# Performance work log

Measured on AMD Instinct MI355X. Metric: run time of the kernel, lower is better.

## Reference

```python
import jax, jax.numpy as jnp
import numpy as np

INPUT_SIZE = 2048
H1 = 256
H2 = 64
NB = 8
BATCH = 16384


def setup_inputs() -> dict:
    key = jax.random.key(0)
    ks = jax.random.split(key, 8)
    x = jax.random.normal(ks[0], (BATCH, INPUT_SIZE), dtype=jnp.float32)
    bucket_indices = jax.random.randint(ks[1], (BATCH,), 0, NB, dtype=jnp.int32)
    # torch nn.Linear weights: (out_features, in_features), bias: (out_features,)
    def lin(k, fan_in, fan_out):
        kw, kb = jax.random.split(k)
        bound = 1.0 / np.sqrt(fan_in)
        W = jax.random.uniform(kw, (fan_out, fan_in), jnp.float32, -bound, bound)
        b = jax.random.uniform(kb, (fan_out,), jnp.float32, -bound, bound)
        return W, b
    W1, b1 = lin(ks[2], INPUT_SIZE, H1 * NB)
    W2, b2 = lin(ks[3], H1, H2 * NB)
    W3, b3 = lin(ks[4], H2, 1 * NB)
    return {"x": x, "bucket_indices": bucket_indices,
            "W1": W1, "b1": b1, "W2": W2, "b2": b2, "W3": W3, "b3": b3}


def _gather_bucket(all_out, idx, width):
    # all_out: (B, NB*width) -> select per-sample bucket slice -> (B, width)
    B = all_out.shape[0]
    per = all_out.reshape(B, NB, width)
    return jnp.take_along_axis(per, idx[:, None, None], axis=1)[:, 0, :]


def reference(x, bucket_indices, W1, b1, W2, b2, W3, b3):
    idx = bucket_indices.astype(jnp.int32)
    h1_all = x @ W1.T + b1                      # (B, H1*NB)
    h1 = jnp.clip(_gather_bucket(h1_all, idx, H1), 0.0, 1.0)
    h2_all = h1 @ W2.T + b2                     # (B, H2*NB)
    h2 = jnp.clip(_gather_bucket(h2_all, idx, H2), 0.0, 1.0)
    out_all = h2 @ W3.T + b3                    # (B, NB)
    out = _gather_bucket(out_all, idx, 1)       # (B, 1)
    return out[:, :, None]                      # (B, 1, 1) matches unsqueeze(-1)
```

## Files before the change

kernel.cpp:

```cpp
#include <hip/hip_runtime.h>

#define INSZ   2048
#define NH1    256
#define NH2    64
#define NB     8
#define BATCH  16384

#define TS        64
#define MAXTILES  (BATCH / TS)
#define GRIDX     (NB * MAXTILES)

#define W1F_U4   (NB * 64 * 16 * 64)
#define W2F_U4   (NB * 8 * 4 * 64)

#define META_OFF  0
#define ORDER_OFF 1024
#define W1F_OFF   (1024 + BATCH * 4)
#define W2F_OFF   (W1F_OFF + W1F_U4 * 16)
#define WS_NEED   (W2F_OFF + W2F_U4 * 16)

typedef float f4  __attribute__((ext_vector_type(4)));
typedef float f32x4 __attribute__((ext_vector_type(4)));
typedef short bf16x8 __attribute__((ext_vector_type(8)));

__device__ __forceinline__ unsigned short f2bf(float f) {
    unsigned u = __float_as_uint(f);
    u += 0x7fffu + ((u >> 16) & 1u);
    return (unsigned short)(u >> 16);
}
__device__ __forceinline__ float clamp01(float v) { return fminf(fmaxf(v, 0.0f), 1.0f); }
__device__ __forceinline__ unsigned pack2(float a, float b) {
    return (unsigned)f2bf(a) | ((unsigned)f2bf(b) << 16);
}

__device__ __forceinline__ void glds16(const short* gsrc, short* ldst) {
    __builtin_amdgcn_global_load_lds(
        (const __attribute__((address_space(1))) unsigned int*)gsrc,
        (__attribute__((address_space(3))) unsigned int*)ldst, 16, 0, 0);
}


__global__ void k_countscan(const int* __restrict__ idx, int* __restrict__ meta) {
    __shared__ int scnt[NB];
    int t = threadIdx.x;
    if (t < NB) scnt[t] = 0;
    __syncthreads();
    int local[NB];
#pragma unroll
    for (int bb = 0; bb < NB; bb++) local[bb] = 0;
    for (int i = t; i < BATCH; i += 1024) {
        int b = idx[i];
#pragma unroll
        for (int bb = 0; bb < NB; bb++) local[bb] += (b == bb) ? 1 : 0;
    }
#pragma unroll
    for (int bb = 0; bb < NB; bb++) {
        int v = local[bb];
        v += __shfl_xor(v, 1);  v += __shfl_xor(v, 2);  v += __shfl_xor(v, 4);
        v += __shfl_xor(v, 8);  v += __shfl_xor(v, 16); v += __shfl_xor(v, 32);
        if ((t & 63) == 0) atomicAdd(&scnt[bb], v);
    }
    __syncthreads();
    if (t == 0) {
        int run = 0;
        for (int b = 0; b < NB; b++) {
            int c = scnt[b];
            meta[b]      = c;
            meta[8 + b]  = run;
            meta[16 + b] = run;
            run += c;
        }
    }
}

__global__ void k_scatter(const int* __restrict__ idx, int* __restrict__ meta,
                          int* __restrict__ order) {
    __shared__ int wcnt[16][NB];
    __shared__ int sbase[NB];
    int t = threadIdx.x;
    int i = blockIdx.x * 1024 + t;
    int b = idx[i];
    int wv = t >> 6, lane = t & 63;
    unsigned long long mymask = 0;
#pragma unroll
    for (int bb = 0; bb < NB; bb++) {
        unsigned long long m = __ballot(b == bb);
        if (b == bb) mymask = m;
        if (lane == bb) wcnt[wv][bb] = (int)__popcll(m);
    }
    int myrank = (int)__popcll(mymask & ((1ull << lane) - 1ull));
    __syncthreads();
    if (t < NB) {
        int sum = 0;
        for (int w2 = 0; w2 < 16; w2++) { int c = wcnt[w2][t]; wcnt[w2][t] = sum; sum += c; }
        sbase[t] = atomicAdd(&meta[16 + t], sum);
    }
    __syncthreads();
    order[sbase[b] + wcnt[wv][b] + myrank] = i;
}

__global__ void k_pack(const float* __restrict__ W1, const float* __restrict__ W2,
                       uint4* __restrict__ W1f, uint4* __restrict__ W2f) {
    int u = blockIdx.x * 256 + threadIdx.x;
    if (u < W1F_U4) {
        int lane = u & 63, cb = (u >> 6) & 15, kb = (u >> 10) & 63, bkt = u >> 16;
        int l15 = lane & 15, quad = lane >> 4;
        const float* p = W1 + (size_t)(bkt * NH1 + cb * 16 + l15) * INSZ + kb * 32 + quad * 8;
        f4 lo = *(const f4*)p, hi = *(const f4*)(p + 4);
        uint4 o;
        o.x = pack2(lo[0], lo[1]); o.y = pack2(lo[2], lo[3]);
        o.z = pack2(hi[0], hi[1]); o.w = pack2(hi[2], hi[3]);
        W1f[u] = o;
    } else {
        int v = u - W1F_U4;
        if (v >= W2F_U4) return;
        int lane = v & 63, cg2 = (v >> 6) & 3, kb2 = (v >> 8) & 7, bkt = v >> 11;
        int l15 = lane & 15, quad = lane >> 4;
        const float* p = W2 + (size_t)(bkt * NH2 + cg2 * 16 + l15) * NH1 + kb2 * 32 + quad * 8;
        f4 lo = *(const f4*)p, hi = *(const f4*)(p + 4);
        uint4 o;
        o.x = pack2(lo[0], lo[1]); o.y = pack2(lo[2], lo[3]);
        o.z = pack2(hi[0], hi[1]); o.w = pack2(hi[2], hi[3]);
        W2f[v] = o;
    }
}


__global__ __launch_bounds__(512, 2) void fused_v6(
    const float* __restrict__ x, const int* __restrict__ meta,
    const int* __restrict__ order,
    const short* __restrict__ W1f, const short* __restrict__ W2f,
    const float* __restrict__ b1, const float* __restrict__ b2,
    const float* __restrict__ W3, const float* __restrict__ b3,
    float* __restrict__ out)
{
    const int bkt  = blockIdx.x & 7;
    const int base = (blockIdx.x >> 3) * TS;
    const int cnt  = meta[bkt];
    if (base >= cnt) return;
    const int off = meta[8 + bkt];

    __shared__ short sW[2][8192];
    __shared__ short sX[2][TS * 40];
    __shared__ short sh1[TS * 264];
    __shared__ float sPart[2][TS];

    const int t = threadIdx.x;
    const int lane = t & 63, w = t >> 6;
    const int l15 = lane & 15, quad = lane >> 4;
    const int g = w & 1, c = w >> 1;

    const int xr = t >> 3, kq = t & 7;
    int ir = base + xr; if (ir > cnt - 1) ir = cnt - 1;
    const float* xtp = x + (size_t)order[off + ir] * INSZ + kq * 4;
    const int sxo = xr * 40 + kq * 4;

    const short* wtile = W1f + ((size_t)bkt << 19);

    f32x4 acc[2][4];
#pragma unroll
    for (int a = 0; a < 2; a++)
#pragma unroll
        for (int i = 0; i < 4; i++) acc[a][i] = (f32x4)0.0f;

    glds16(wtile + (2 * w)     * 512 + lane * 8, &sW[0][(2 * w)     * 512]);
    glds16(wtile + (2 * w + 1) * 512 + lane * 8, &sW[0][(2 * w + 1) * 512]);
    {
        f4 xv = *(const f4*)xtp;
        uint2 pk; pk.x = pack2(xv[0], xv[1]); pk.y = pack2(xv[2], xv[3]);
        *(uint2*)&sX[0][sxo] = pk;
    }
    __syncthreads();

#pragma unroll 1
    for (int kb = 0; kb < 64; kb++) {
        const int p = kb & 1;
        f4 xn;
        if (kb < 63) {
            const short* gw = wtile + (size_t)(kb + 1) * 8192;
            glds16(gw + (2 * w)     * 512 + lane * 8, &sW[p ^ 1][(2 * w)     * 512]);
            glds16(gw + (2 * w + 1) * 512 + lane * 8, &sW[p ^ 1][(2 * w + 1) * 512]);
            xn = *(const f4*)(xtp + (kb + 1) * 32);
        }

        bf16x8 a0 = *(const bf16x8*)&sX[p][(g * 32 + l15)      * 40 + quad * 8];
        bf16x8 a1 = *(const bf16x8*)&sX[p][(g * 32 + 16 + l15) * 40 + quad * 8];
#pragma unroll
        for (int i = 0; i < 4; i++) {
            bf16x8 bf = *(const bf16x8*)&sW[p][((c * 4 + i) * 64 + lane) * 8];
            acc[0][i] = __builtin_amdgcn_mfma_f32_16x16x32_bf16(a0, bf, acc[0][i], 0, 0, 0);
            acc[1][i] = __builtin_amdgcn_mfma_f32_16x16x32_bf16(a1, bf, acc[1][i], 0, 0, 0);
        }

        if (kb < 63) {
            uint2 pk; pk.x = pack2(xn[0], xn[1]); pk.y = pack2(xn[2], xn[3]);
            *(uint2*)&sX[p ^ 1][sxo] = pk;
        }
        __syncthreads();
    }

#pragma unroll
    for (int i = 0; i < 4; i++) {
        int col = c * 64 + i * 16 + l15;
        float bias = b1[bkt * NH1 + col];
#pragma unroll
        for (int a = 0; a < 2; a++)
#pragma unroll
            for (int r = 0; r < 4; r++) {
                int row = g * 32 + a * 16 + quad * 4 + r;
                sh1[row * 264 + col] = (short)f2bf(clamp01(acc[a][i][r] + bias));
            }
    }
    __syncthreads();

    const int rw = w & 3, ch2 = w >> 2;
    f32x4 c2[2];
    c2[0] = (f32x4)0.0f; c2[1] = (f32x4)0.0f;
    const short* w2p = W2f + (size_t)bkt * 16384 + lane * 8;
#pragma unroll
    for (int kb2 = 0; kb2 < 8; kb2++) {
        bf16x8 a2 = *(const bf16x8*)&sh1[(rw * 16 + l15) * 264 + kb2 * 32 + quad * 8];
#pragma unroll
        for (int j = 0; j < 2; j++) {
            bf16x8 bw = *(const bf16x8*)(w2p + (kb2 * 4 + ch2 * 2 + j) * 512);
            c2[j] = __builtin_amdgcn_mfma_f32_16x16x32_bf16(a2, bw, c2[j], 0, 0, 0);
        }
    }

    float s[4] = {0, 0, 0, 0};
#pragma unroll
    for (int j = 0; j < 2; j++) {
        int n2 = (ch2 * 2 + j) * 16 + l15;
        float bias2 = b2[bkt * NH2 + n2];
        float w3v   = W3[bkt * NH2 + n2];
#pragma unroll
        for (int r = 0; r < 4; r++)
            s[r] += clamp01(c2[j][r] + bias2) * w3v;
    }
#pragma unroll
    for (int r = 0; r < 4; r++) {
        float pp = s[r];
        pp += __shfl_xor(pp, 1); pp += __shfl_xor(pp, 2);
        pp += __shfl_xor(pp, 4); pp += __shfl_xor(pp, 8);
        if (l15 == 0) sPart[ch2][rw * 16 + quad * 4 + r] = pp;
    }
    __syncthreads();
    if (t < TS && base + t < cnt)
        out[order[off + base + t]] = sPart[0][t] + sPart[1][t] + b3[bkt];
}


__global__ void naive_mlp(const float* __restrict__ x, const int* __restrict__ idx,
                          const float* __restrict__ W1, const float* __restrict__ b1,
                          const float* __restrict__ W2, const float* __restrict__ b2,
                          const float* __restrict__ W3, const float* __restrict__ b3,
                          float* __restrict__ out)
{
    int i = blockIdx.x;
    int b = idx[i];
    __shared__ float sx[INSZ];
    __shared__ float sh1n[NH1];
    __shared__ float sh2n[NH2];
    for (int t = threadIdx.x; t < INSZ; t += 256) sx[t] = x[(size_t)i * INSZ + t];
    __syncthreads();
    int j = threadIdx.x;
    {
        const float* wr = W1 + (size_t)(b * NH1 + j) * INSZ;
        float acc = b1[b * NH1 + j];
        for (int k = 0; k < INSZ; k++) acc += sx[k] * wr[k];
        sh1n[j] = fminf(fmaxf(acc, 0.f), 1.f);
    }
    __syncthreads();
    if (j < NH2) {
        const float* wr = W2 + (size_t)(b * NH2 + j) * NH1;
        float acc = b2[b * NH2 + j];
        for (int k = 0; k < NH1; k++) acc += sh1n[k] * wr[k];
        sh2n[j] = fminf(fmaxf(acc, 0.f), 1.f);
    }
    __syncthreads();
    if (j == 0) {
        float acc = b3[b];
        for (int k = 0; k < NH2; k++) acc += sh2n[k] * W3[b * NH2 + k];
        out[i] = acc;
    }
}

extern "C" void kernel_launch(void* const* d_in, const int* in_sizes, int n_in,
                              void* d_out, int out_size, void* d_ws, size_t ws_size,
                              hipStream_t stream) {
    const float* x  = (const float*)d_in[0];
    const int* bidx = (const int*)d_in[1];
    const float* W1 = (const float*)d_in[2];
    const float* b1 = (const float*)d_in[3];
    const float* W2 = (const float*)d_in[4];
    const float* b2 = (const float*)d_in[5];
    const float* W3 = (const float*)d_in[6];
    const float* b3 = (const float*)d_in[7];
    float* out = (float*)d_out;

    if (ws_size >= (size_t)WS_NEED) {
        char* ws = (char*)d_ws;
        int*   meta  = (int*)(ws + META_OFF);
        int*   order = (int*)(ws + ORDER_OFF);
        uint4* W1f   = (uint4*)(ws + W1F_OFF);
        uint4* W2f   = (uint4*)(ws + W2F_OFF);

        k_countscan<<<1, 1024, 0, stream>>>(bidx, meta);
        k_scatter<<<BATCH / 1024, 1024, 0, stream>>>(bidx, meta, order);
        k_pack<<<(W1F_U4 + W2F_U4) / 256, 256, 0, stream>>>(W1, W2, W1f, W2f);
        fused_v6<<<GRIDX, 512, 0, stream>>>(x, meta, order,
                                            (const short*)W1f, (const short*)W2f,
                                            b1, b2, W3, b3, out);
    } else {
        naive_mlp<<<BATCH, 256, 0, stream>>>(x, bidx, W1, b1, W2, b2, W3, b3, out);
    }
}
```

Before: 271.9 us.

## Load W1 fragments directly into registers and remap tile order

The layer-1 weight tiles are no longer staged through LDS with global_load_lds. Each wave now loads its own W1 fragments straight into registers with a register double buffer, and the X tile is prefetched two steps ahead. Waves are repartitioned so each owns all 64 rows and 32 output columns, which removes the shared weight buffer and half the LDS reads per MFMA step. Block-to-tile mapping is also swizzled so that concurrently running blocks of a bucket are spread out. The cost is more registers and a hand-placed waitcnt/barrier sequence.

```diff
diff --git a/kernel.cpp b/kernel.cpp
--- a/kernel.cpp
+++ b/kernel.cpp
@@ -31,12 +31,6 @@
 __device__ __forceinline__ float clamp01(float v) { return fminf(fmaxf(v, 0.0f), 1.0f); }
 __device__ __forceinline__ unsigned pack2(float a, float b) {
     return (unsigned)f2bf(a) | ((unsigned)f2bf(b) << 16);
-}
-
-__device__ __forceinline__ void glds16(const short* gsrc, short* ldst) {
-    __builtin_amdgcn_global_load_lds(
-        (const __attribute__((address_space(1))) unsigned int*)gsrc,
-        (__attribute__((address_space(3))) unsigned int*)ldst, 16, 0, 0);
 }
 
 
@@ -126,7 +120,7 @@
 }
 
 
-__global__ __launch_bounds__(512, 2) void fused_v6(
+__global__ __launch_bounds__(512, 2) void fused_v7(
     const float* __restrict__ x, const int* __restrict__ meta,
     const int* __restrict__ order,
     const short* __restrict__ W1f, const short* __restrict__ W2f,
@@ -135,12 +129,13 @@
     float* __restrict__ out)
 {
     const int bkt  = blockIdx.x & 7;
-    const int base = (blockIdx.x >> 3) * TS;
+    const int u    = blockIdx.x >> 3;
+    const int tile = ((u & 7) << 5) | (u >> 3);
     const int cnt  = meta[bkt];
+    const int base = tile * TS;
     if (base >= cnt) return;
     const int off = meta[8 + bkt];
 
-    __shared__ short sW[2][8192];
     __shared__ short sX[2][TS * 40];
     __shared__ short sh1[TS * 264];
     __shared__ float sPart[2][TS];
@@ -148,67 +143,77 @@
     const int t = threadIdx.x;
     const int lane = t & 63, w = t >> 6;
     const int l15 = lane & 15, quad = lane >> 4;
-    const int g = w & 1, c = w >> 1;
 
     const int xr = t >> 3, kq = t & 7;
     int ir = base + xr; if (ir > cnt - 1) ir = cnt - 1;
     const float* xtp = x + (size_t)order[off + ir] * INSZ + kq * 4;
     const int sxo = xr * 40 + kq * 4;
 
-    const short* wtile = W1f + ((size_t)bkt << 19);
-
-    f32x4 acc[2][4];
-#pragma unroll
-    for (int a = 0; a < 2; a++)
-#pragma unroll
-        for (int i = 0; i < 4; i++) acc[a][i] = (f32x4)0.0f;
-
-    glds16(wtile + (2 * w)     * 512 + lane * 8, &sW[0][(2 * w)     * 512]);
-    glds16(wtile + (2 * w + 1) * 512 + lane * 8, &sW[0][(2 * w + 1) * 512]);
+    const short* wp = W1f + ((size_t)bkt << 19) + (size_t)(2 * w) * 512 + lane * 8;
+
+    f32x4 acc[4][2];
+#pragma unroll
+    for (int f = 0; f < 4; f++)
+#pragma unroll
+        for (int j = 0; j < 2; j++) acc[f][j] = (f32x4)0.0f;
+
+    bf16x8 wA0, wA1, wB0, wB1;
+    f4 xs0, xs1;
+
+    wA0 = *(const bf16x8*)(wp);
+    wA1 = *(const bf16x8*)(wp + 512);
     {
-        f4 xv = *(const f4*)xtp;
-        uint2 pk; pk.x = pack2(xv[0], xv[1]); pk.y = pack2(xv[2], xv[3]);
+        f4 x0 = *(const f4*)xtp;
+        xs1 = *(const f4*)(xtp + 32);
+        uint2 pk; pk.x = pack2(x0[0], x0[1]); pk.y = pack2(x0[2], x0[3]);
         *(uint2*)&sX[0][sxo] = pk;
     }
-    __syncthreads();
+
+#define L1_STEP(KB, P, WU0, WU1, WL0, WL1, XW, XL)                                      \
+    {                                                                                   \
+        asm volatile("s_waitcnt lgkmcnt(0)" ::: "memory");                              \
+        __builtin_amdgcn_s_barrier();                                                   \
+        asm volatile("" ::: "memory");                                                  \
+        if ((KB) < 63) {                                                                \
+            WL0 = *(const bf16x8*)(wp + (size_t)((KB) + 1) * 8192);                     \
+            WL1 = *(const bf16x8*)(wp + (size_t)((KB) + 1) * 8192 + 512);               \
+        }                                                                               \
+        if ((KB) < 62) XL = *(const f4*)(xtp + ((KB) + 2) * 32);                        \
+        bf16x8 a0 = *(const bf16x8*)&sX[P][(l15)      * 40 + quad * 8];                 \
+        bf16x8 a1 = *(const bf16x8*)&sX[P][(16 + l15) * 40 + quad * 8];                 \
+        bf16x8 a2 = *(const bf16x8*)&sX[P][(32 + l15) * 40 + quad * 8];                 \
+        bf16x8 a3 = *(const bf16x8*)&sX[P][(48 + l15) * 40 + quad * 8];                 \
+        acc[0][0] = __builtin_amdgcn_mfma_f32_16x16x32_bf16(a0, WU0, acc[0][0], 0,0,0); \
+        acc[0][1] = __builtin_amdgcn_mfma_f32_16x16x32_bf16(a0, WU1, acc[0][1], 0,0,0); \
+        acc[1][0] = __builtin_amdgcn_mfma_f32_16x16x32_bf16(a1, WU0, acc[1][0], 0,0,0); \
+        acc[1][1] = __builtin_amdgcn_mfma_f32_16x16x32_bf16(a1, WU1, acc[1][1], 0,0,0); \
+        acc[2][0] = __builtin_amdgcn_mfma_f32_16x16x32_bf16(a2, WU0, acc[2][0], 0,0,0); \
+        acc[2][1] = __builtin_amdgcn_mfma_f32_16x16x32_bf16(a2, WU1, acc[2][1], 0,0,0); \
+        acc[3][0] = __builtin_amdgcn_mfma_f32_16x16x32_bf16(a3, WU0, acc[3][0], 0,0,0); \
+        acc[3][1] = __builtin_amdgcn_mfma_f32_16x16x32_bf16(a3, WU1, acc[3][1], 0,0,0); \
+        if ((KB) < 63) {                                                                \
+            uint2 pk; pk.x = pack2(XW[0], XW[1]); pk.y = pack2(XW[2], XW[3]);           \
+            *(uint2*)&sX[(P) ^ 1][sxo] = pk;                                            \
+        }                                                                               \
+    }
 
 #pragma unroll 1
-    for (int kb = 0; kb < 64; kb++) {
-        const int p = kb & 1;
-        f4 xn;
-        if (kb < 63) {
-            const short* gw = wtile + (size_t)(kb + 1) * 8192;
-            glds16(gw + (2 * w)     * 512 + lane * 8, &sW[p ^ 1][(2 * w)     * 512]);
-            glds16(gw + (2 * w + 1) * 512 + lane * 8, &sW[p ^ 1][(2 * w + 1) * 512]);
-            xn = *(const f4*)(xtp + (kb + 1) * 32);
-        }
-
-        bf16x8 a0 = *(const bf16x8*)&sX[p][(g * 32 + l15)      * 40 + quad * 8];
-        bf16x8 a1 = *(const bf16x8*)&sX[p][(g * 32 + 16 + l15) * 40 + quad * 8];
-#pragma unroll
-        for (int i = 0; i < 4; i++) {
-            bf16x8 bf = *(const bf16x8*)&sW[p][((c * 4 + i) * 64 + lane) * 8];
-            acc[0][i] = __builtin_amdgcn_mfma_f32_16x16x32_bf16(a0, bf, acc[0][i], 0, 0, 0);
-            acc[1][i] = __builtin_amdgcn_mfma_f32_16x16x32_bf16(a1, bf, acc[1][i], 0, 0, 0);
-        }
-
-        if (kb < 63) {
-            uint2 pk; pk.x = pack2(xn[0], xn[1]); pk.y = pack2(xn[2], xn[3]);
-            *(uint2*)&sX[p ^ 1][sxo] = pk;
-        }
-        __syncthreads();
-    }
-
-#pragma unroll
-    for (int i = 0; i < 4; i++) {
-        int col = c * 64 + i * 16 + l15;
+    for (int kb = 0; kb < 64; kb += 2) {
+        L1_STEP(kb,     0, wA0, wA1, wB0, wB1, xs1, xs0)
+        L1_STEP(kb + 1, 1, wB0, wB1, wA0, wA1, xs0, xs1)
+    }
+#undef L1_STEP
+
+#pragma unroll
+    for (int j = 0; j < 2; j++) {
+        int col = w * 32 + j * 16 + l15;
         float bias = b1[bkt * NH1 + col];
 #pragma unroll
-        for (int a = 0; a < 2; a++)
+        for (int f = 0; f < 4; f++)
 #pragma unroll
             for (int r = 0; r < 4; r++) {
-                int row = g * 32 + a * 16 + quad * 4 + r;
-                sh1[row * 264 + col] = (short)f2bf(clamp01(acc[a][i][r] + bias));
+                int row = f * 16 + quad * 4 + r;
+                sh1[row * 264 + col] = (short)f2bf(clamp01(acc[f][j][r] + bias));
             }
     }
     __syncthreads();
@@ -308,7 +313,7 @@
         k_countscan<<<1, 1024, 0, stream>>>(bidx, meta);
         k_scatter<<<BATCH / 1024, 1024, 0, stream>>>(bidx, meta, order);
         k_pack<<<(W1F_U4 + W2F_U4) / 256, 256, 0, stream>>>(W1, W2, W1f, W2f);
-        fused_v6<<<GRIDX, 512, 0, stream>>>(x, meta, order,
+        fused_v7<<<GRIDX, 512, 0, stream>>>(x, meta, order,
                                             (const short*)W1f, (const short*)W2f,
                                             b1, b2, W3, b3, out);
     } else {
```

New measurement: 337.4 us. +24.1%, slower.

## Stream W1 fragments to registers and pipeline fp32 x tiles through swizzled LDS

Applied to the files above, without the earlier changes.

Layer-1 weight fragments now go straight from global memory into registers, double-buffered two k-steps ahead, instead of being staged through LDS. The x rows are copied as fp32 into a four-deep XOR-swizzled LDS ring with global_load_lds and converted to bf16 at MFMA operand time. Synchronisation uses explicit vmcnt waits and bare s_barrier rather than __syncthreads. The pack kernel is reordered so its reads of W1/W2 are coalesced, and biases are hoisted into registers at kernel start. This aims to overlap load latency with MFMA work, at the cost of more register pressure and fragile hand-counted waitcnt values.

```diff
diff --git a/kernel.cpp b/kernel.cpp
--- a/kernel.cpp
+++ b/kernel.cpp
@@ -31,12 +31,6 @@
 __device__ __forceinline__ float clamp01(float v) { return fminf(fmaxf(v, 0.0f), 1.0f); }
 __device__ __forceinline__ unsigned pack2(float a, float b) {
     return (unsigned)f2bf(a) | ((unsigned)f2bf(b) << 16);
-}
-
-__device__ __forceinline__ void glds16(const short* gsrc, short* ldst) {
-    __builtin_amdgcn_global_load_lds(
-        (const __attribute__((address_space(1))) unsigned int*)gsrc,
-        (__attribute__((address_space(3))) unsigned int*)ldst, 16, 0, 0);
 }
 
 
@@ -103,30 +97,38 @@
                        uint4* __restrict__ W1f, uint4* __restrict__ W2f) {
     int u = blockIdx.x * 256 + threadIdx.x;
     if (u < W1F_U4) {
-        int lane = u & 63, cb = (u >> 6) & 15, kb = (u >> 10) & 63, bkt = u >> 16;
-        int l15 = lane & 15, quad = lane >> 4;
-        const float* p = W1 + (size_t)(bkt * NH1 + cb * 16 + l15) * INSZ + kb * 32 + quad * 8;
+        int k8 = u & 255, row = (u >> 8) & 255, bkt = u >> 16;
+        int kb = k8 >> 2, quad = k8 & 3;
+        int cb = row >> 4, l15 = row & 15;
+        const float* p = W1 + ((size_t)(bkt * NH1 + row)) * INSZ + k8 * 8;
         f4 lo = *(const f4*)p, hi = *(const f4*)(p + 4);
         uint4 o;
         o.x = pack2(lo[0], lo[1]); o.y = pack2(lo[2], lo[3]);
         o.z = pack2(hi[0], hi[1]); o.w = pack2(hi[2], hi[3]);
-        W1f[u] = o;
+        W1f[((bkt * 64 + kb) * 16 + cb) * 64 + quad * 16 + l15] = o;
     } else {
         int v = u - W1F_U4;
         if (v >= W2F_U4) return;
-        int lane = v & 63, cg2 = (v >> 6) & 3, kb2 = (v >> 8) & 7, bkt = v >> 11;
-        int l15 = lane & 15, quad = lane >> 4;
-        const float* p = W2 + (size_t)(bkt * NH2 + cg2 * 16 + l15) * NH1 + kb2 * 32 + quad * 8;
+        int k8 = v & 31, row = (v >> 5) & 63, bkt = v >> 11;
+        int kb2 = k8 >> 2, quad = k8 & 3;
+        int cg2 = row >> 4, l15 = row & 15;
+        const float* p = W2 + ((size_t)(bkt * NH2 + row)) * NH1 + k8 * 8;
         f4 lo = *(const f4*)p, hi = *(const f4*)(p + 4);
         uint4 o;
         o.x = pack2(lo[0], lo[1]); o.y = pack2(lo[2], lo[3]);
         o.z = pack2(hi[0], hi[1]); o.w = pack2(hi[2], hi[3]);
-        W2f[v] = o;
-    }
-}
-
-
-__global__ __launch_bounds__(512, 2) void fused_v6(
+        W2f[((bkt * 8 + kb2) * 4 + cg2) * 64 + quad * 16 + l15] = o;
+    }
+}
+
+
+#define MFMA16 __builtin_amdgcn_mfma_f32_16x16x32_bf16
+#define WLD(D, P) asm volatile("global_load_dwordx4 %0, %1, off" : "=&v"(D) : "v"(P))
+#define GLDS16(SRC, DST) __builtin_amdgcn_global_load_lds( \
+    (const __attribute__((address_space(1))) unsigned int*)(SRC), \
+    (__attribute__((address_space(3))) unsigned int*)(DST), 16, 0, 0)
+
+__global__ __launch_bounds__(512, 2) void fused_v12(
     const float* __restrict__ x, const int* __restrict__ meta,
     const int* __restrict__ order,
     const short* __restrict__ W1f, const short* __restrict__ W2f,
@@ -135,27 +137,46 @@
     float* __restrict__ out)
 {
     const int bkt  = blockIdx.x & 7;
-    const int base = (blockIdx.x >> 3) * TS;
+    const int tile = blockIdx.x >> 3;
     const int cnt  = meta[bkt];
+    const int base = tile * TS;
     if (base >= cnt) return;
     const int off = meta[8 + bkt];
 
-    __shared__ short sW[2][8192];
-    __shared__ short sX[2][TS * 40];
+    __shared__ float sXf[4][2048];
     __shared__ short sh1[TS * 264];
     __shared__ float sPart[2][TS];
 
     const int t = threadIdx.x;
     const int lane = t & 63, w = t >> 6;
     const int l15 = lane & 15, quad = lane >> 4;
-    const int g = w & 1, c = w >> 1;
-
-    const int xr = t >> 3, kq = t & 7;
-    int ir = base + xr; if (ir > cnt - 1) ir = cnt - 1;
-    const float* xtp = x + (size_t)order[off + ir] * INSZ + kq * 4;
-    const int sxo = xr * 40 + kq * 4;
-
-    const short* wtile = W1f + ((size_t)bkt << 19);
+    const int g = w & 1, c4 = w >> 1;
+
+    const int srow = lane >> 3, sj = (lane & 7) ^ srow;
+    int sir = base + w * 8 + srow; if (sir > cnt - 1) sir = cnt - 1;
+    const float* xsl = x + (size_t)order[off + sir] * INSZ + sj * 4;
+    float* ldst = &sXf[0][0] + w * 256;
+
+    const int rho = l15 & 7;
+    const int grp0 = (g * 32 + l15) >> 3, grp1 = (g * 32 + 16 + l15) >> 3;
+    const int cl = (((2 * quad) ^ rho) << 4), ch = (((2 * quad + 1) ^ rho) << 4);
+    const int oa0l = grp0 * 1024 + rho * 128 + cl, oa0h = grp0 * 1024 + rho * 128 + ch;
+    const int oa1l = grp1 * 1024 + rho * 128 + cl, oa1h = grp1 * 1024 + rho * 128 + ch;
+
+    const short* wp = W1f + ((size_t)bkt << 19) + (size_t)(c4 * 4) * 512 + lane * 8;
+
+    const int rw = w & 3, ch2 = w >> 2;
+    float b1v0 = b1[bkt * NH1 + c4 * 64 + 0 * 16 + l15];
+    float b1v1 = b1[bkt * NH1 + c4 * 64 + 1 * 16 + l15];
+    float b1v2 = b1[bkt * NH1 + c4 * 64 + 2 * 16 + l15];
+    float b1v3 = b1[bkt * NH1 + c4 * 64 + 3 * 16 + l15];
+    float b2v0 = b2[bkt * NH2 + (ch2 * 2 + 0) * 16 + l15];
+    float b2v1 = b2[bkt * NH2 + (ch2 * 2 + 1) * 16 + l15];
+    float w3v0 = W3[bkt * NH2 + (ch2 * 2 + 0) * 16 + l15];
+    float w3v1 = W3[bkt * NH2 + (ch2 * 2 + 1) * 16 + l15];
+    float b3v  = b3[bkt];
+    asm volatile("" :: "v"(b1v0), "v"(b1v1), "v"(b1v2), "v"(b1v3),
+                       "v"(b2v0), "v"(b2v1), "v"(w3v0), "v"(w3v1), "v"(b3v));
 
     f32x4 acc[2][4];
 #pragma unroll
@@ -163,57 +184,82 @@
 #pragma unroll
         for (int i = 0; i < 4; i++) acc[a][i] = (f32x4)0.0f;
 
-    glds16(wtile + (2 * w)     * 512 + lane * 8, &sW[0][(2 * w)     * 512]);
-    glds16(wtile + (2 * w + 1) * 512 + lane * 8, &sW[0][(2 * w + 1) * 512]);
+    bf16x8 wa0, wa1, wa2, wa3, wb0, wb1, wb2, wb3;
+
+    WLD(wa0, wp);            WLD(wa1, wp + 512);
+    WLD(wa2, wp + 1024);     WLD(wa3, wp + 1536);
+    GLDS16(xsl, ldst);
     {
-        f4 xv = *(const f4*)xtp;
-        uint2 pk; pk.x = pack2(xv[0], xv[1]); pk.y = pack2(xv[2], xv[3]);
-        *(uint2*)&sX[0][sxo] = pk;
-    }
-    __syncthreads();
+        const short* wq = wp + 8192;
+        WLD(wb0, wq);        WLD(wb1, wq + 512);
+        WLD(wb2, wq + 1024); WLD(wb3, wq + 1536);
+    }
+    GLDS16(xsl + 32, ldst + 2048);
+    GLDS16(xsl + 64, ldst + 4096);
+    asm volatile("s_waitcnt vmcnt(6)");
+    __builtin_amdgcn_s_barrier();
+    __builtin_amdgcn_sched_barrier(0);
+
+#define L1_STEP(KB, BUF, GBUF, W0, W1, W2, W3r, DOW, DOG, VMW)                          \
+    {                                                                                   \
+        const char* sb = (const char*)&sXf[BUF][0];                                     \
+        f4 l0 = *(const f4*)(sb + oa0l), h0 = *(const f4*)(sb + oa0h);                  \
+        f4 l1 = *(const f4*)(sb + oa1l), h1 = *(const f4*)(sb + oa1h);                  \
+        bf16x8 a0, a1;                                                                  \
+        { uint4 u; u.x = pack2(l0[0], l0[1]); u.y = pack2(l0[2], l0[3]);                \
+          u.z = pack2(h0[0], h0[1]); u.w = pack2(h0[2], h0[3]);                         \
+          a0 = *(bf16x8*)&u; }                                                          \
+        { uint4 u; u.x = pack2(l1[0], l1[1]); u.y = pack2(l1[2], l1[3]);                \
+          u.z = pack2(h1[0], h1[1]); u.w = pack2(h1[2], h1[3]);                         \
+          a1 = *(bf16x8*)&u; }                                                          \
+        acc[0][0] = MFMA16(a0, W0, acc[0][0], 0, 0, 0);                                 \
+        acc[0][1] = MFMA16(a0, W1, acc[0][1], 0, 0, 0);                                 \
+        acc[0][2] = MFMA16(a0, W2, acc[0][2], 0, 0, 0);                                 \
+        acc[0][3] = MFMA16(a0, W3r, acc[0][3], 0, 0, 0);                                \
+        acc[1][0] = MFMA16(a1, W0, acc[1][0], 0, 0, 0);                                 \
+        acc[1][1] = MFMA16(a1, W1, acc[1][1], 0, 0, 0);                                 \
+        acc[1][2] = MFMA16(a1, W2, acc[1][2], 0, 0, 0);                                 \
+        acc[1][3] = MFMA16(a1, W3r, acc[1][3], 0, 0, 0);                                \
+        if (DOW) {                                                                      \
+            const short* wq = wp + (size_t)((KB) + 2) * 8192;                           \
+            WLD(W0, wq);        WLD(W1, wq + 512);                                      \
+            WLD(W2, wq + 1024); WLD(W3r, wq + 1536);                                    \
+        }                                                                               \
+        if (DOG) GLDS16(xsl + (size_t)((KB) + 3) * 32, ldst + (GBUF) * 2048);           \
+        asm volatile("s_waitcnt vmcnt(" #VMW ")");                                      \
+        __builtin_amdgcn_s_barrier();                                                   \
+        __builtin_amdgcn_sched_barrier(0);                                              \
+    }
 
 #pragma unroll 1
-    for (int kb = 0; kb < 64; kb++) {
-        const int p = kb & 1;
-        f4 xn;
-        if (kb < 63) {
-            const short* gw = wtile + (size_t)(kb + 1) * 8192;
-            glds16(gw + (2 * w)     * 512 + lane * 8, &sW[p ^ 1][(2 * w)     * 512]);
-            glds16(gw + (2 * w + 1) * 512 + lane * 8, &sW[p ^ 1][(2 * w + 1) * 512]);
-            xn = *(const f4*)(xtp + (kb + 1) * 32);
+    for (int kbb = 0; kbb < 60; kbb += 4) {
+        L1_STEP(kbb + 0, 0, 3, wa0, wa1, wa2, wa3, 1, 1, 6)
+        L1_STEP(kbb + 1, 1, 0, wb0, wb1, wb2, wb3, 1, 1, 6)
+        L1_STEP(kbb + 2, 2, 1, wa0, wa1, wa2, wa3, 1, 1, 6)
+        L1_STEP(kbb + 3, 3, 2, wb0, wb1, wb2, wb3, 1, 1, 6)
+    }
+    L1_STEP(60, 0, 3, wa0, wa1, wa2, wa3, 1, 1, 6)
+    L1_STEP(61, 1, 0, wb0, wb1, wb2, wb3, 1, 0, 5)
+    L1_STEP(62, 2, 0, wa0, wa1, wa2, wa3, 0, 0, 0)
+    L1_STEP(63, 3, 0, wb0, wb1, wb2, wb3, 0, 0, 0)
+#undef L1_STEP
+
+    {
+        float b1v[4] = {b1v0, b1v1, b1v2, b1v3};
+#pragma unroll
+        for (int i = 0; i < 4; i++) {
+            int col = c4 * 64 + i * 16 + l15;
+#pragma unroll
+            for (int a = 0; a < 2; a++)
+#pragma unroll
+                for (int r = 0; r < 4; r++) {
+                    int row = g * 32 + a * 16 + quad * 4 + r;
+                    sh1[row * 264 + col] = (short)f2bf(clamp01(acc[a][i][r] + b1v[i]));
+                }
         }
-
-        bf16x8 a0 = *(const bf16x8*)&sX[p][(g * 32 + l15)      * 40 + quad * 8];
-        bf16x8 a1 = *(const bf16x8*)&sX[p][(g * 32 + 16 + l15) * 40 + quad * 8];
-#pragma unroll
-        for (int i = 0; i < 4; i++) {
-            bf16x8 bf = *(const bf16x8*)&sW[p][((c * 4 + i) * 64 + lane) * 8];
-            acc[0][i] = __builtin_amdgcn_mfma_f32_16x16x32_bf16(a0, bf, acc[0][i], 0, 0, 0);
-            acc[1][i] = __builtin_amdgcn_mfma_f32_16x16x32_bf16(a1, bf, acc[1][i], 0, 0, 0);
-        }
-
-        if (kb < 63) {
-            uint2 pk; pk.x = pack2(xn[0], xn[1]); pk.y = pack2(xn[2], xn[3]);
-            *(uint2*)&sX[p ^ 1][sxo] = pk;
-        }
-        __syncthreads();
-    }
-
-#pragma unroll
-    for (int i = 0; i < 4; i++) {
-        int col = c * 64 + i * 16 + l15;
-        float bias = b1[bkt * NH1 + col];
-#pragma unroll
-        for (int a = 0; a < 2; a++)
-#pragma unroll
-            for (int r = 0; r < 4; r++) {
-                int row = g * 32 + a * 16 + quad * 4 + r;
-                sh1[row * 264 + col] = (short)f2bf(clamp01(acc[a][i][r] + bias));
-            }
-    }
-    __syncthreads();
-
-    const int rw = w & 3, ch2 = w >> 2;
+    }
+    __syncthreads();
+
     f32x4 c2[2];
     c2[0] = (f32x4)0.0f; c2[1] = (f32x4)0.0f;
     const short* w2p = W2f + (size_t)bkt * 16384 + lane * 8;
@@ -223,19 +269,15 @@
 #pragma unroll
         for (int j = 0; j < 2; j++) {
             bf16x8 bw = *(const bf16x8*)(w2p + (kb2 * 4 + ch2 * 2 + j) * 512);
-            c2[j] = __builtin_amdgcn_mfma_f32_16x16x32_bf16(a2, bw, c2[j], 0, 0, 0);
+            c2[j] = MFMA16(a2, bw, c2[j], 0, 0, 0);
         }
     }
 
     float s[4] = {0, 0, 0, 0};
 #pragma unroll
-    for (int j = 0; j < 2; j++) {
-        int n2 = (ch2 * 2 + j) * 16 + l15;
-        float bias2 = b2[bkt * NH2 + n2];
-        float w3v   = W3[bkt * NH2 + n2];
-#pragma unroll
-        for (int r = 0; r < 4; r++)
-            s[r] += clamp01(c2[j][r] + bias2) * w3v;
+    for (int r = 0; r < 4; r++) {
+        s[r] += clamp01(c2[0][r] + b2v0) * w3v0;
+        s[r] += clamp01(c2[1][r] + b2v1) * w3v1;
     }
 #pragma unroll
     for (int r = 0; r < 4; r++) {
@@ -246,7 +288,7 @@
     }
     __syncthreads();
     if (t < TS && base + t < cnt)
-        out[order[off + base + t]] = sPart[0][t] + sPart[1][t] + b3[bkt];
+        out[order[off + base + t]] = sPart[0][t] + sPart[1][t] + b3v;
 }
 
 
@@ -308,9 +350,9 @@
         k_countscan<<<1, 1024, 0, stream>>>(bidx, meta);
         k_scatter<<<BATCH / 1024, 1024, 0, stream>>>(bidx, meta, order);
         k_pack<<<(W1F_U4 + W2F_U4) / 256, 256, 0, stream>>>(W1, W2, W1f, W2f);
-        fused_v6<<<GRIDX, 512, 0, stream>>>(x, meta, order,
-                                            (const short*)W1f, (const short*)W2f,
-                                            b1, b2, W3, b3, out);
+        fused_v12<<<GRIDX, 512, 0, stream>>>(x, meta, order,
+                                             (const short*)W1f, (const short*)W2f,
+                                             b1, b2, W3, b3, out);
     } else {
         naive_mlp<<<BATCH, 256, 0, stream>>>(x, bidx, W1, b1, W2, b2, W3, b3, out);
     }
```

Result: slower. 279.0 us (+2.6%).
